# Kernel tuning notes

Hardware: AMD Instinct MI355X
Metric: run time of the kernel (lower is better)

Reference implementation:

```python
import jax, jax.numpy as jnp
import numpy as np

B, L, INPUT_DIM = 4, 4096, 32
D_MODEL, N_LAYERS = 256, 2
D_STATE, D_CONV, EXPAND = 16, 4, 2
D_INNER = EXPAND * D_MODEL          # 512
DT_RANK = (D_MODEL + 15) // 16      # 16
OUTPUT_DIM, HORIZON = 32, 4
LN_EPS = 1e-5


def setup_inputs() -> dict:
    key = jax.random.key(0)
    ks = jax.random.split(key, 16)
    s = 0.02
    inp = {
        "x": jax.random.normal(ks[0], (B, L, INPUT_DIM), jnp.float32),
        "enc_w": jax.random.normal(ks[1], (D_MODEL, INPUT_DIM), jnp.float32) * s,
        "enc_b": jnp.zeros((D_MODEL,), jnp.float32),
        "in_proj_w": jax.random.normal(ks[2], (N_LAYERS, 2 * D_INNER, D_MODEL), jnp.float32) * s,
        "conv_w": jax.random.normal(ks[3], (N_LAYERS, D_INNER, D_CONV), jnp.float32) * s,
        "conv_b": jnp.zeros((N_LAYERS, D_INNER), jnp.float32),
        "xproj_w": jax.random.normal(ks[4], (N_LAYERS, DT_RANK + 2 * D_STATE, D_INNER), jnp.float32) * s,
        "dtproj_w": jax.random.normal(ks[5], (N_LAYERS, D_INNER, DT_RANK), jnp.float32) * s,
        "dtproj_b": jax.random.normal(ks[6], (N_LAYERS, D_INNER), jnp.float32) * 0.1,
        "A_log": jnp.log(jnp.tile(jnp.arange(1.0, D_STATE + 1.0, dtype=jnp.float32), (N_LAYERS, D_INNER, 1))),
        "Dp": jnp.ones((N_LAYERS, D_INNER), jnp.float32),
        "out_proj_w": jax.random.normal(ks[7], (N_LAYERS, D_MODEL, D_INNER), jnp.float32) * s,
        "ln_g": jnp.ones((D_MODEL,), jnp.float32),
        "ln_b": jnp.zeros((D_MODEL,), jnp.float32),
        "head_w": jax.random.normal(ks[8], (OUTPUT_DIM * HORIZON, D_MODEL), jnp.float32) * s,
        "head_b": jnp.zeros((OUTPUT_DIM * HORIZON,), jnp.float32),
    }
    return inp


def _mamba_block(x, in_w, cw, cb, xp_w, dt_w, dt_b, A_log, Dp, out_w):
    # x: [B, L, d_model]
    b, l, _ = x.shape
    xz = jnp.einsum("bld,ed->ble", x, in_w)            # [B, L, 2*d_inner]
    xi, res = jnp.split(xz, 2, axis=-1)
    # causal depthwise conv1d (padding=d_conv-1, truncated to L)
    xpad = jnp.pad(xi, ((0, 0), (D_CONV - 1, 0), (0, 0)))
    xi = sum(xpad[:, k:k + l, :] * cw[:, k] for k in range(D_CONV)) + cb
    xi = jax.nn.silu(xi)
    dbl = jnp.einsum("bld,ed->ble", xi, xp_w)           # [B, L, dt_rank+2*d_state]
    dt = dbl[..., :DT_RANK]
    Bm = dbl[..., DT_RANK:DT_RANK + D_STATE]            # [B, L, d_state]
    Cm = dbl[..., DT_RANK + D_STATE:]                   # [B, L, d_state]
    dt = jax.nn.softplus(jnp.einsum("blr,dr->bld", dt, dt_w) + dt_b)  # [B, L, d_inner]
    A = -jnp.exp(A_log)                                 # [d_inner, d_state]

    def step(h, ins):
        dt_t, B_t, C_t, x_t = ins                       # [B,di],[B,ds],[B,ds],[B,di]
        dA = jnp.exp(dt_t[..., None] * A)               # [B, d_inner, d_state]
        h = dA * h + (dt_t * x_t)[..., None] * B_t[:, None, :]
        y = jnp.einsum("bds,bs->bd", h, C_t)
        return h, y

    h0 = jnp.zeros((b, D_INNER, D_STATE), x.dtype)
    xs = (jnp.moveaxis(dt, 1, 0), jnp.moveaxis(Bm, 1, 0),
          jnp.moveaxis(Cm, 1, 0), jnp.moveaxis(xi, 1, 0))
    _, ys = jax.lax.scan(step, h0, xs)                  # ys: [L, B, d_inner]
    y = jnp.moveaxis(ys, 0, 1) + xi * Dp
    y = y * jax.nn.silu(res)
    return jnp.einsum("ble,de->bld", y, out_w)


def reference(x, enc_w, enc_b, in_proj_w, conv_w, conv_b, xproj_w, dtproj_w,
              dtproj_b, A_log, Dp, out_proj_w, ln_g, ln_b, head_w, head_b):
    h = jnp.einsum("bli,di->bld", x, enc_w) + enc_b     # encoder
    for i in range(N_LAYERS):
        h = h + _mamba_block(h, in_proj_w[i], conv_w[i], conv_b[i], xproj_w[i],
                             dtproj_w[i], dtproj_b[i], A_log[i], Dp[i], out_proj_w[i])
    mu = jnp.mean(h, axis=-1, keepdims=True)
    var = jnp.mean((h - mu) ** 2, axis=-1, keepdims=True)
    hn = (h - mu) * jax.lax.rsqrt(var + LN_EPS) * ln_g + ln_b
    state = hn[:, -1, :]                                # last timestep
    return jnp.einsum("bd,od->bo", state, head_w) + head_b
```

## Files before the change

kernel.cpp:

```cpp
#include <hip/hip_runtime.h>
#include <hip/hip_bf16.h>
#include <math.h>

#define BB 4
#define LL 4096
#define DM 256
#define DI 512
#define DS 16
#define NOUTK 128
#define LN_EPS 1e-5f
#define NC 128
#define CLEN (LL/NC)
#define BL (BB*LL)
#define LDB 640

typedef __attribute__((ext_vector_type(8))) short short8;
typedef __attribute__((ext_vector_type(4))) float f32x4;

__device__ __forceinline__ ushort f2bf(float f) {
    union { float f; unsigned u; } v; v.f = f;
    unsigned r = (v.u + 0x7FFF + ((v.u >> 16) & 1)) >> 16;
    return (ushort)r;
}
__device__ __forceinline__ float bf2f(ushort u) {
    union { unsigned u; float f; } v; v.u = ((unsigned)u) << 16;
    return v.f;
}

#define PREP_N1 (2*1024*256)
#define PREP_N2 (2*256*512)
#define PREP_N3 (2*640*512)
__global__ __launch_bounds__(256) void prep_kernel(
    const float* __restrict__ inw, const float* __restrict__ opw,
    const float* __restrict__ xpw, const float* __restrict__ dtw,
    ushort* __restrict__ inw_bf, ushort* __restrict__ opw_bf,
    ushort* __restrict__ comb_bf)
{
    int i = blockIdx.x * 256 + threadIdx.x;
    if (i < PREP_N1) {
        inw_bf[i] = f2bf(inw[i]);
        return;
    }
    int j = i - PREP_N1;
    if (j < PREP_N2) {
        opw_bf[j] = f2bf(opw[j]);
        return;
    }
    int m = j - PREP_N2;
    if (m >= PREP_N3) return;
    int l = m / (640 * 512);
    int rem = m - l * 640 * 512;
    int row = rem >> 9, k = rem & 511;
    const float* xp = xpw + l * 48 * 512;
    const float* dw = dtw + l * 512 * 16;
    float v;
    if (row < 512) {
        v = 0.f;
        #pragma unroll
        for (int r = 0; r < 16; ++r)
            v = fmaf(dw[row * 16 + r], xp[r * 512 + k], v);
    } else if (row < 544) {
        v = xp[(row - 512 + 16) * 512 + k];
    } else v = 0.f;
    comb_bf[m] = f2bf(v);
}

__global__ __launch_bounds__(256) void enc_kernel(
    const float* __restrict__ x, const float* __restrict__ w,
    const float* __restrict__ b, ushort* __restrict__ hbf)
{
    __shared__ float sw[256 * 33];
    __shared__ float sx[4][32];
    int tid = threadIdx.x;
    for (int i = tid; i < 256 * 8; i += 256) {
        float4 v = ((const float4*)w)[i];
        int r = i >> 3, c = (i & 7) * 4;
        sw[r * 33 + c + 0] = v.x; sw[r * 33 + c + 1] = v.y;
        sw[r * 33 + c + 2] = v.z; sw[r * 33 + c + 3] = v.w;
    }
    int row0 = blockIdx.x * 4;
    if (tid < 32) {
        for (int rr = 0; rr < 4; ++rr)
            sx[rr][tid] = x[(size_t)(row0 + rr) * 32 + tid];
    }
    __syncthreads();
    float bb = b[tid];
    #pragma unroll
    for (int rr = 0; rr < 4; ++rr) {
        float acc = bb;
        #pragma unroll
        for (int k = 0; k < 32; ++k)
            acc = fmaf(sx[rr][k], sw[tid * 33 + k], acc);
        hbf[(size_t)(row0 + rr) * DM + tid] = f2bf(acc);
    }
}

template<int EPI>
__global__ __launch_bounds__(256, 4) void mfma_gemm(
    const ushort* __restrict__ A, int lda,
    const ushort* __restrict__ W,
    const float* __restrict__ bias,
    float* __restrict__ C, int ldc,
    ushort* Cbf, int ldcbf,
    int K)
{
    __shared__ ushort As[64 * 64];
    __shared__ ushort Ws[128 * 64];
    const int tid = threadIdx.x;

    int nwg = gridDim.x * gridDim.y;
    int wlin = blockIdx.y * gridDim.x + blockIdx.x;
    int gx = blockIdx.x, gy = blockIdx.y;
    if ((nwg & 7) == 0) {
        int q = nwg >> 3;
        int s = (wlin & 7) * q + (wlin >> 3);
        gx = s % gridDim.x;
        gy = s / gridDim.x;
    }
    const int bm = gy * 64;
    const int bn = gx * 128;
    const int wid = tid >> 6, lane = tid & 63;
    const int wrow = (wid >> 1) * 32, wcol = (wid & 1) * 64;
    const int sr = tid >> 3;
    const int sc = tid & 7;

    f32x4 acc[2][4];
    #pragma unroll
    for (int mi = 0; mi < 2; ++mi)
        #pragma unroll
        for (int ni = 0; ni < 4; ++ni)
            acc[mi][ni] = (f32x4){0.f, 0.f, 0.f, 0.f};

    const int nk = K >> 6;
    for (int t = 0; t < nk; ++t) {
        const int k0 = t << 6;
        #pragma unroll
        for (int it = 0; it < 2; ++it) {
            int r = it * 32 + sr;
            int csrc = sc ^ (r & 7);
            __builtin_amdgcn_global_load_lds(
                (const __attribute__((address_space(1))) unsigned int*)
                    (A + (size_t)(bm + r) * lda + k0 + csrc * 8),
                (__attribute__((address_space(3))) unsigned int*)
                    (As + r * 64 + sc * 8), 16, 0, 0);
        }
        #pragma unroll
        for (int it = 0; it < 4; ++it) {
            int r = it * 32 + sr;
            int csrc = sc ^ (r & 7);
            __builtin_amdgcn_global_load_lds(
                (const __attribute__((address_space(1))) unsigned int*)
                    (W + (size_t)(bn + r) * K + k0 + csrc * 8),
                (__attribute__((address_space(3))) unsigned int*)
                    (Ws + r * 64 + sc * 8), 16, 0, 0);
        }
        __syncthreads();
        #pragma unroll
        for (int kk = 0; kk < 2; ++kk) {
            short8 af[2], bfr[4];
            #pragma unroll
            for (int mi = 0; mi < 2; ++mi) {
                int r = wrow + mi * 16 + (lane & 15);
                int c = (lane >> 4) + kk * 4;
                af[mi] = *(const short8*)(As + r * 64 + ((c ^ (r & 7)) << 3));
            }
            #pragma unroll
            for (int ni = 0; ni < 4; ++ni) {
                int r = wcol + ni * 16 + (lane & 15);
                int c = (lane >> 4) + kk * 4;
                bfr[ni] = *(const short8*)(Ws + r * 64 + ((c ^ (r & 7)) << 3));
            }
            #pragma unroll
            for (int mi = 0; mi < 2; ++mi)
                #pragma unroll
                for (int ni = 0; ni < 4; ++ni)
                    acc[mi][ni] = __builtin_amdgcn_mfma_f32_16x16x32_bf16(
                        af[mi], bfr[ni], acc[mi][ni], 0, 0, 0);
        }
        __syncthreads();
    }

    #pragma unroll
    for (int mi = 0; mi < 2; ++mi)
        #pragma unroll
        for (int ni = 0; ni < 4; ++ni) {
            int col = bn + wcol + ni * 16 + (lane & 15);
            #pragma unroll
            for (int r = 0; r < 4; ++r) {
                int row = bm + wrow + mi * 16 + (lane >> 4) * 4 + r;
                float v = acc[mi][ni][r];
                if (EPI == 1) {
                    if (col < 512) {
                        float u = v + bias[col];
                        float sp = fmaxf(u, 0.f) + __logf(1.f + __expf(-fabsf(u)));
                        Cbf[(size_t)row * ldcbf + col] = f2bf(sp);
                    } else if (col < 544) {
                        C[(size_t)row * ldc + (col - 512)] = v;
                    }
                } else if (EPI == 2) {
                    size_t o = (size_t)row * ldcbf + col;
                    float vv = v + bf2f(Cbf[o]);
                    Cbf[o] = f2bf(vv);
                } else {
                    Cbf[(size_t)row * ldcbf + col] = f2bf(v);
                }
            }
        }
}

__global__ __launch_bounds__(256) void conv_silu_kernel(
    const ushort* __restrict__ xz, const float* __restrict__ cw,
    const float* __restrict__ cb, ushort* __restrict__ xi)
{
    int idx = blockIdx.x * 256 + threadIdx.x;
    int d4 = (idx & 127) * 4;
    int grp = idx >> 7;
    int b = grp >> 9;
    int t0 = (grp & 511) * 8;
    const ushort* base = xz + ((size_t)(b * LL + t0) * 1024) + d4;
    ushort* obase = xi + ((size_t)(b * LL + t0) * 512) + d4;

    float4 w0 = *(const float4*)(cw + (d4 + 0) * 4);
    float4 w1 = *(const float4*)(cw + (d4 + 1) * 4);
    float4 w2 = *(const float4*)(cw + (d4 + 2) * 4);
    float4 w3 = *(const float4*)(cw + (d4 + 3) * 4);
    float b0 = cb[d4 + 0], b1 = cb[d4 + 1], b2 = cb[d4 + 2], b3 = cb[d4 + 3];

    ushort4 z4 = {0, 0, 0, 0};
    ushort4 win0 = (t0 >= 3) ? *(const ushort4*)(base - 3 * 1024) : z4;
    ushort4 win1 = (t0 >= 2) ? *(const ushort4*)(base - 2 * 1024) : z4;
    ushort4 win2 = (t0 >= 1) ? *(const ushort4*)(base - 1 * 1024) : z4;

    #pragma unroll
    for (int k = 0; k < 8; ++k) {
        ushort4 cur = *(const ushort4*)(base + k * 1024);
        float a0 = b0, a1 = b1, a2 = b2, a3 = b3;
        a0 = fmaf(bf2f(win0.x), w0.x, a0); a1 = fmaf(bf2f(win0.y), w1.x, a1);
        a2 = fmaf(bf2f(win0.z), w2.x, a2); a3 = fmaf(bf2f(win0.w), w3.x, a3);
        a0 = fmaf(bf2f(win1.x), w0.y, a0); a1 = fmaf(bf2f(win1.y), w1.y, a1);
        a2 = fmaf(bf2f(win1.z), w2.y, a2); a3 = fmaf(bf2f(win1.w), w3.y, a3);
        a0 = fmaf(bf2f(win2.x), w0.z, a0); a1 = fmaf(bf2f(win2.y), w1.z, a1);
        a2 = fmaf(bf2f(win2.z), w2.z, a2); a3 = fmaf(bf2f(win2.w), w3.z, a3);
        a0 = fmaf(bf2f(cur.x),  w0.w, a0); a1 = fmaf(bf2f(cur.y),  w1.w, a1);
        a2 = fmaf(bf2f(cur.z),  w2.w, a2); a3 = fmaf(bf2f(cur.w),  w3.w, a3);
        ushort4 o;
        o.x = f2bf(a0 / (1.f + __expf(-a0)));
        o.y = f2bf(a1 / (1.f + __expf(-a1)));
        o.z = f2bf(a2 / (1.f + __expf(-a2)));
        o.w = f2bf(a3 / (1.f + __expf(-a3)));
        *(ushort4*)(obase + k * 512) = o;
        win0 = win1; win1 = win2; win2 = cur;
    }
}

__global__ __launch_bounds__(256) void scan_phase1(
    const ushort* __restrict__ xi, const ushort* __restrict__ dtb,
    const float* __restrict__ bc,
    const float* __restrict__ alog,
    float* __restrict__ cS, float* __restrict__ cH)
{
    int d = blockIdx.z * 256 + threadIdx.x;
    int b = blockIdx.y, c = blockIdx.x;
    float Av[16];
    bool fast = true;
    #pragma unroll
    for (int s = 0; s < 16; ++s) {
        Av[s] = -__expf(alog[d * 16 + s]);
        fast = fast && (fabsf(Av[s] + (float)(s + 1)) < 1e-3f * (s + 1));
    }
    float h[16];
    #pragma unroll
    for (int s = 0; s < 16; ++s) h[s] = 0.f;
    float S = 0.f;
    int t0 = c * CLEN;
    if (fast) {
        for (int t = t0; t < t0 + CLEN; ++t) {
            size_t row = (size_t)b * LL + t;
            float dt = bf2f(dtb[row * 512 + d]);
            float x = bf2f(xi[row * 512 + d]);
            float dtx = dt * x;
            S += dt;
            const float* bp = bc + row * 32;
            float e1 = __expf(-dt);
            float e2=e1*e1, e3=e2*e1, e4=e2*e2, e5=e3*e2, e6=e3*e3, e7=e4*e3, e8=e4*e4;
            float e9=e5*e4, e10=e5*e5, e11=e6*e5, e12=e6*e6, e13=e7*e6, e14=e7*e7, e15=e8*e7, e16=e8*e8;
            float pw[16] = {e1,e2,e3,e4,e5,e6,e7,e8,e9,e10,e11,e12,e13,e14,e15,e16};
            #pragma unroll
            for (int s = 0; s < 16; ++s)
                h[s] = fmaf(pw[s], h[s], dtx * bp[s]);
        }
    } else {
        for (int t = t0; t < t0 + CLEN; ++t) {
            size_t row = (size_t)b * LL + t;
            float dt = bf2f(dtb[row * 512 + d]);
            float x = bf2f(xi[row * 512 + d]);
            float dtx = dt * x;
            S += dt;
            const float* bp = bc + row * 32;
            #pragma unroll
            for (int s = 0; s < 16; ++s) {
                float dA = __expf(dt * Av[s]);
                h[s] = fmaf(dA, h[s], dtx * bp[s]);
            }
        }
    }
    cS[((size_t)b * DI + d) * NC + c] = S;
    size_t base = (((size_t)b * DI + d) * NC + c) * 16;
    #pragma unroll
    for (int q = 0; q < 4; ++q)
        *(float4*)(cH + base + q*4) = *(float4*)&h[q*4];
}

__global__ __launch_bounds__(256) void scan_phase2(
    const float* __restrict__ cS, float* __restrict__ cH,
    const float* __restrict__ alog)
{
    int bd = blockIdx.x;
    int d = bd & (DI - 1);
    int tid = threadIdx.x;
    int s = tid >> 4;
    int g = tid & 15;
    float Avs = -__expf(alog[d * 16 + s]);
    size_t sbase = (size_t)bd * NC;
    size_t base = (size_t)bd * NC * 16 + s;
    float a8[8], h8[8];
    #pragma unroll
    for (int j = 0; j < 8; ++j) {
        float Sj = cS[sbase + g * 8 + j];
        a8[j] = __expf(Avs * Sj);
        h8[j] = cH[base + (size_t)(g * 8 + j) * 16];
    }
    float A = 1.f, H = 0.f;
    #pragma unroll
    for (int j = 0; j < 8; ++j) {
        H = fmaf(a8[j], H, h8[j]);
        A *= a8[j];
    }
    #pragma unroll
    for (int off = 1; off < 16; off <<= 1) {
        float Ap = __shfl_up(A, off, 16);
        float Hp = __shfl_up(H, off, 16);
        if (g >= off) { H = fmaf(A, Hp, H); A *= Ap; }
    }
    float init = __shfl_up(H, 1, 16);
    if (g == 0) init = 0.f;
    #pragma unroll
    for (int j = 0; j < 8; ++j) {
        size_t o = base + (size_t)(g * 8 + j) * 16;
        cH[o] = init;
        init = fmaf(a8[j], init, h8[j]);
    }
}

__global__ __launch_bounds__(256) void scan_phase3(
    const ushort* __restrict__ xz,
    ushort* __restrict__ xi,
    const ushort* __restrict__ dtb,
    const float* __restrict__ bc,
    const float* __restrict__ alog,
    const float* __restrict__ Dp,
    const float* __restrict__ cH,
    int c0)
{
    int d = blockIdx.z * 256 + threadIdx.x;
    int b = blockIdx.y;
    int c = blockIdx.x + c0;
    float Av[16];
    bool fast = true;
    #pragma unroll
    for (int s = 0; s < 16; ++s) {
        Av[s] = -__expf(alog[d * 16 + s]);
        fast = fast && (fabsf(Av[s] + (float)(s + 1)) < 1e-3f * (s + 1));
    }
    float h[16];
    size_t cbase = (((size_t)b * DI + d) * NC + c) * 16;
    #pragma unroll
    for (int q = 0; q < 4; ++q)
        *(float4*)&h[q*4] = *(const float4*)(cH + cbase + q*4);
    float Dd = Dp[d];
    int t0 = c * CLEN;
    if (fast) {
        for (int t = t0; t < t0 + CLEN; ++t) {
            size_t row = (size_t)b * LL + t;
            float dt = bf2f(dtb[row * 512 + d]);
            float x = bf2f(xi[row * 512 + d]);
            float dtx = dt * x;
            const float* bp = bc + row * 32;
            const float* cp = bc + row * 32 + 16;
            float e1 = __expf(-dt);
            float e2=e1*e1, e3=e2*e1, e4=e2*e2, e5=e3*e2, e6=e3*e3, e7=e4*e3, e8=e4*e4;
            float e9=e5*e4, e10=e5*e5, e11=e6*e5, e12=e6*e6, e13=e7*e6, e14=e7*e7, e15=e8*e7, e16=e8*e8;
            float pw[16] = {e1,e2,e3,e4,e5,e6,e7,e8,e9,e10,e11,e12,e13,e14,e15,e16};
            float y = 0.f;
            #pragma unroll
            for (int s = 0; s < 16; ++s) {
                h[s] = fmaf(pw[s], h[s], dtx * bp[s]);
                y = fmaf(h[s], cp[s], y);
            }
            float res = bf2f(xz[row * 1024 + 512 + d]);
            float g = (y + x * Dd) * (res / (1.f + __expf(-res)));
            xi[row * 512 + d] = f2bf(g);
        }
    } else {
        for (int t = t0; t < t0 + CLEN; ++t) {
            size_t row = (size_t)b * LL + t;
            float dt = bf2f(dtb[row * 512 + d]);
            float x = bf2f(xi[row * 512 + d]);
            float dtx = dt * x;
            const float* bp = bc + row * 32;
            const float* cp = bc + row * 32 + 16;
            float y = 0.f;
            #pragma unroll
            for (int s = 0; s < 16; ++s) {
                float dA = __expf(dt * Av[s]);
                h[s] = fmaf(dA, h[s], dtx * bp[s]);
                y = fmaf(h[s], cp[s], y);
            }
            float res = bf2f(xz[row * 1024 + 512 + d]);
            float g = (y + x * Dd) * (res / (1.f + __expf(-res)));
            xi[row * 512 + d] = f2bf(g);
        }
    }
}

__global__ __launch_bounds__(256) void out_proj_last_kernel(
    const ushort* __restrict__ xi, const float* __restrict__ W,
    const ushort* __restrict__ hbf, float* __restrict__ hlast)
{
    int b = blockIdx.x, n = threadIdx.x;
    __shared__ float sy[DI];
    const ushort* yrow = xi + ((size_t)b * LL + (LL - 1)) * DI;
    for (int k = threadIdx.x; k < DI; k += 256) sy[k] = bf2f(yrow[k]);
    __syncthreads();
    const float* wr = W + (size_t)n * DI;
    float acc = 0.f;
    for (int k = 0; k < DI; k += 4) {
        float4 wv = *(const float4*)(wr + k);
        acc = fmaf(sy[k+0], wv.x, acc);
        acc = fmaf(sy[k+1], wv.y, acc);
        acc = fmaf(sy[k+2], wv.z, acc);
        acc = fmaf(sy[k+3], wv.w, acc);
    }
    hlast[b * DM + n] = acc + bf2f(hbf[((size_t)b * LL + (LL - 1)) * DM + n]);
}

__global__ __launch_bounds__(256) void ln_head_kernel(
    const float* __restrict__ hlast, const float* __restrict__ lng,
    const float* __restrict__ lnb, const float* __restrict__ hw,
    const float* __restrict__ hb, float* __restrict__ out)
{
    int b = blockIdx.x, tid = threadIdx.x;
    __shared__ float sh[DM];
    __shared__ float r1[4], r2[4];
    float v = hlast[b * DM + tid];
    float s = v;
    #pragma unroll
    for (int o = 32; o >= 1; o >>= 1) s += __shfl_down(s, o);
    if ((tid & 63) == 0) r1[tid >> 6] = s;
    __syncthreads();
    float mu = (r1[0] + r1[1] + r1[2] + r1[3]) * (1.f / 256.f);
    float dv = v - mu;
    float q = dv * dv;
    #pragma unroll
    for (int o = 32; o >= 1; o >>= 1) q += __shfl_down(q, o);
    if ((tid & 63) == 0) r2[tid >> 6] = q;
    __syncthreads();
    float var = (r2[0] + r2[1] + r2[2] + r2[3]) * (1.f / 256.f);
    sh[tid] = dv * rsqrtf(var + LN_EPS) * lng[tid] + lnb[tid];
    __syncthreads();
    if (tid < NOUTK) {
        const float* wr = hw + (size_t)tid * DM;
        float acc = hb[tid];
        for (int d2 = 0; d2 < DM; d2 += 4) {
            float4 wv = *(const float4*)(wr + d2);
            acc = fmaf(sh[d2+0], wv.x, acc);
            acc = fmaf(sh[d2+1], wv.y, acc);
            acc = fmaf(sh[d2+2], wv.z, acc);
            acc = fmaf(sh[d2+3], wv.w, acc);
        }
        out[b * NOUTK + tid] = acc;
    }
}

extern "C" void kernel_launch(void* const* d_in, const int* in_sizes, int n_in,
                              void* d_out, int out_size, void* d_ws, size_t ws_size,
                              hipStream_t stream)
{
    const float* x    = (const float*)d_in[0];
    const float* encw = (const float*)d_in[1];
    const float* encb = (const float*)d_in[2];
    const float* inw  = (const float*)d_in[3];
    const float* cw   = (const float*)d_in[4];
    const float* cb   = (const float*)d_in[5];
    const float* xpw  = (const float*)d_in[6];
    const float* dtw  = (const float*)d_in[7];
    const float* dtb  = (const float*)d_in[8];
    const float* alog = (const float*)d_in[9];
    const float* Dp   = (const float*)d_in[10];
    const float* opw  = (const float*)d_in[11];
    const float* lng  = (const float*)d_in[12];
    const float* lnb  = (const float*)d_in[13];
    const float* hw   = (const float*)d_in[14];
    const float* hb   = (const float*)d_in[15];
    float* out = (float*)d_out;

    float* ws   = (float*)d_ws;
    float* bc   = ws;
    float* cS   = bc  + (size_t)BL * 32;
    float* cH   = cS  + (size_t)BB * DI * NC;
    float* hlast = cH + (size_t)BB * DI * NC * DS;
    ushort* h_bf    = (ushort*)(hlast + BB * DM);
    ushort* xz_bf   = h_bf  + (size_t)BL * DM;
    ushort* xi_bf   = xz_bf + (size_t)BL * 1024;
    ushort* dt_bf   = xi_bf + (size_t)BL * DI;
    ushort* inw_bf  = dt_bf + (size_t)BL * DI;
    ushort* opw_bf  = inw_bf + 2 * 1024 * DM;
    ushort* comb_bf = opw_bf + 2 * DM * DI;

    dim3 blk(256, 1, 1);

    prep_kernel<<<dim3((PREP_N1 + PREP_N2 + PREP_N3) / 256), blk, 0, stream>>>(
        inw, opw, xpw, dtw, inw_bf, opw_bf, comb_bf);

    enc_kernel<<<dim3(BL/4), blk, 0, stream>>>(x, encw, encb, h_bf);

    for (int l = 0; l < 2; ++l) {
        mfma_gemm<0><<<dim3(1024/128, BL/64), blk, 0, stream>>>(
            h_bf, DM, inw_bf + (size_t)l * 1024 * DM, nullptr,
            nullptr, 0, xz_bf, 1024, DM);
        conv_silu_kernel<<<dim3(BL * 128 / 8 / 256), blk, 0, stream>>>(
            xz_bf, cw + l * DI * 4, cb + l * DI, xi_bf);
        mfma_gemm<1><<<dim3(LDB/128, BL/64), blk, 0, stream>>>(
            xi_bf, DI, comb_bf + (size_t)l * LDB * DI, dtb + l * DI,
            bc, 32, dt_bf, 512, DI);
        scan_phase1<<<dim3(NC, BB, 2), blk, 0, stream>>>(
            xi_bf, dt_bf, bc, alog + (size_t)l * DI * 16, cS, cH);
        scan_phase2<<<dim3(BB * DI), blk, 0, stream>>>(
            cS, cH, alog + (size_t)l * DI * 16);
        if (l == 0) {
            scan_phase3<<<dim3(NC, BB, 2), blk, 0, stream>>>(
                xz_bf, xi_bf, dt_bf, bc, alog + (size_t)l * DI * 16,
                Dp + l * DI, cH, 0);
            mfma_gemm<2><<<dim3(DM/128, BL/64), blk, 0, stream>>>(
                xi_bf, DI, opw_bf + (size_t)l * DM * DI, nullptr,
                nullptr, 0, h_bf, DM, DI);
        } else {
            scan_phase3<<<dim3(1, BB, 2), blk, 0, stream>>>(
                xz_bf, xi_bf, dt_bf, bc, alog + (size_t)l * DI * 16,
                Dp + l * DI, cH, NC - 1);
            out_proj_last_kernel<<<dim3(BB), blk, 0, stream>>>(
                xi_bf, opw + (size_t)l * DM * DI, h_bf, hlast);
        }
    }

    ln_head_kernel<<<dim3(BB), blk, 0, stream>>>(hlast, lng, lnb, hw, hb, out);
}
```

Measured before the change: 306.6 us.

## Load GEMM fragments directly from global memory, dropping LDS staging

The MFMA GEMM no longer stages A and W tiles through LDS with swizzled global_load_lds and barriers. Each wave now reads its bf16 MFMA fragments straight from global memory, and the K loop is fully unrolled through a template parameter. This removes the LDS traffic and the __syncthreads barriers, and the occupancy hint is dropped from launch_bounds. In exchange, tiles shared between waves are reloaded, relying on L1/L2 hits, and the per-lane 16-byte loads with row strides may coalesce less well.

```diff
diff --git a/kernel.cpp b/kernel.cpp
--- a/kernel.cpp
+++ b/kernel.cpp
@@ -95,17 +95,14 @@
     }
 }
 
-template<int EPI>
-__global__ __launch_bounds__(256, 4) void mfma_gemm(
+template<int EPI, int KK>
+__global__ __launch_bounds__(256) void mfma_gemm(
     const ushort* __restrict__ A, int lda,
     const ushort* __restrict__ W,
     const float* __restrict__ bias,
     float* __restrict__ C, int ldc,
-    ushort* Cbf, int ldcbf,
-    int K)
-{
-    __shared__ ushort As[64 * 64];
-    __shared__ ushort Ws[128 * 64];
+    ushort* Cbf, int ldcbf)
+{
     const int tid = threadIdx.x;
 
     int nwg = gridDim.x * gridDim.y;
@@ -121,8 +118,8 @@
     const int bn = gx * 128;
     const int wid = tid >> 6, lane = tid & 63;
     const int wrow = (wid >> 1) * 32, wcol = (wid & 1) * 64;
-    const int sr = tid >> 3;
-    const int sc = tid & 7;
+    const int lr = lane & 15;
+    const int lc = (lane >> 4) * 8;
 
     f32x4 acc[2][4];
     #pragma unroll
@@ -131,53 +128,30 @@
         for (int ni = 0; ni < 4; ++ni)
             acc[mi][ni] = (f32x4){0.f, 0.f, 0.f, 0.f};
 
-    const int nk = K >> 6;
-    for (int t = 0; t < nk; ++t) {
-        const int k0 = t << 6;
-        #pragma unroll
-        for (int it = 0; it < 2; ++it) {
-            int r = it * 32 + sr;
-            int csrc = sc ^ (r & 7);
-            __builtin_amdgcn_global_load_lds(
-                (const __attribute__((address_space(1))) unsigned int*)
-                    (A + (size_t)(bm + r) * lda + k0 + csrc * 8),
-                (__attribute__((address_space(3))) unsigned int*)
-                    (As + r * 64 + sc * 8), 16, 0, 0);
-        }
-        #pragma unroll
-        for (int it = 0; it < 4; ++it) {
-            int r = it * 32 + sr;
-            int csrc = sc ^ (r & 7);
-            __builtin_amdgcn_global_load_lds(
-                (const __attribute__((address_space(1))) unsigned int*)
-                    (W + (size_t)(bn + r) * K + k0 + csrc * 8),
-                (__attribute__((address_space(3))) unsigned int*)
-                    (Ws + r * 64 + sc * 8), 16, 0, 0);
-        }
-        __syncthreads();
-        #pragma unroll
-        for (int kk = 0; kk < 2; ++kk) {
-            short8 af[2], bfr[4];
-            #pragma unroll
-            for (int mi = 0; mi < 2; ++mi) {
-                int r = wrow + mi * 16 + (lane & 15);
-                int c = (lane >> 4) + kk * 4;
-                af[mi] = *(const short8*)(As + r * 64 + ((c ^ (r & 7)) << 3));
-            }
-            #pragma unroll
-            for (int ni = 0; ni < 4; ++ni) {
-                int r = wcol + ni * 16 + (lane & 15);
-                int c = (lane >> 4) + kk * 4;
-                bfr[ni] = *(const short8*)(Ws + r * 64 + ((c ^ (r & 7)) << 3));
-            }
-            #pragma unroll
-            for (int mi = 0; mi < 2; ++mi)
-                #pragma unroll
-                for (int ni = 0; ni < 4; ++ni)
-                    acc[mi][ni] = __builtin_amdgcn_mfma_f32_16x16x32_bf16(
-                        af[mi], bfr[ni], acc[mi][ni], 0, 0, 0);
-        }
-        __syncthreads();
+    const ushort* a0 = A + (size_t)(bm + wrow + lr) * lda + lc;
+    const ushort* a1 = a0 + (size_t)16 * lda;
+    const ushort* w0 = W + (size_t)(bn + wcol + lr) * KK + lc;
+    const ushort* w1 = w0 + 16 * KK;
+    const ushort* w2 = w0 + 32 * KK;
+    const ushort* w3 = w0 + 48 * KK;
+
+    #pragma unroll
+    for (int ks = 0; ks < KK / 32; ++ks) {
+        const int ko = ks * 32;
+        short8 af0 = *(const short8*)(a0 + ko);
+        short8 af1 = *(const short8*)(a1 + ko);
+        short8 b0  = *(const short8*)(w0 + ko);
+        short8 b1  = *(const short8*)(w1 + ko);
+        short8 b2  = *(const short8*)(w2 + ko);
+        short8 b3  = *(const short8*)(w3 + ko);
+        acc[0][0] = __builtin_amdgcn_mfma_f32_16x16x32_bf16(af0, b0, acc[0][0], 0, 0, 0);
+        acc[0][1] = __builtin_amdgcn_mfma_f32_16x16x32_bf16(af0, b1, acc[0][1], 0, 0, 0);
+        acc[0][2] = __builtin_amdgcn_mfma_f32_16x16x32_bf16(af0, b2, acc[0][2], 0, 0, 0);
+        acc[0][3] = __builtin_amdgcn_mfma_f32_16x16x32_bf16(af0, b3, acc[0][3], 0, 0, 0);
+        acc[1][0] = __builtin_amdgcn_mfma_f32_16x16x32_bf16(af1, b0, acc[1][0], 0, 0, 0);
+        acc[1][1] = __builtin_amdgcn_mfma_f32_16x16x32_bf16(af1, b1, acc[1][1], 0, 0, 0);
+        acc[1][2] = __builtin_amdgcn_mfma_f32_16x16x32_bf16(af1, b2, acc[1][2], 0, 0, 0);
+        acc[1][3] = __builtin_amdgcn_mfma_f32_16x16x32_bf16(af1, b3, acc[1][3], 0, 0, 0);
     }
 
     #pragma unroll
@@ -525,14 +499,14 @@
     enc_kernel<<<dim3(BL/4), blk, 0, stream>>>(x, encw, encb, h_bf);
 
     for (int l = 0; l < 2; ++l) {
-        mfma_gemm<0><<<dim3(1024/128, BL/64), blk, 0, stream>>>(
+        mfma_gemm<0, DM><<<dim3(1024/128, BL/64), blk, 0, stream>>>(
             h_bf, DM, inw_bf + (size_t)l * 1024 * DM, nullptr,
-            nullptr, 0, xz_bf, 1024, DM);
+            nullptr, 0, xz_bf, 1024);
         conv_silu_kernel<<<dim3(BL * 128 / 8 / 256), blk, 0, stream>>>(
             xz_bf, cw + l * DI * 4, cb + l * DI, xi_bf);
-        mfma_gemm<1><<<dim3(LDB/128, BL/64), blk, 0, stream>>>(
+        mfma_gemm<1, DI><<<dim3(LDB/128, BL/64), blk, 0, stream>>>(
             xi_bf, DI, comb_bf + (size_t)l * LDB * DI, dtb + l * DI,
-            bc, 32, dt_bf, 512, DI);
+            bc, 32, dt_bf, 512);
         scan_phase1<<<dim3(NC, BB, 2), blk, 0, stream>>>(
             xi_bf, dt_bf, bc, alog + (size_t)l * DI * 16, cS, cH);
         scan_phase2<<<dim3(BB * DI), blk, 0, stream>>>(
@@ -541,9 +515,9 @@
             scan_phase3<<<dim3(NC, BB, 2), blk, 0, stream>>>(
                 xz_bf, xi_bf, dt_bf, bc, alog + (size_t)l * DI * 16,
                 Dp + l * DI, cH, 0);
-            mfma_gemm<2><<<dim3(DM/128, BL/64), blk, 0, stream>>>(
+            mfma_gemm<2, DI><<<dim3(DM/128, BL/64), blk, 0, stream>>>(
                 xi_bf, DI, opw_bf + (size_t)l * DM * DI, nullptr,
-                nullptr, 0, h_bf, DM, DI);
+                nullptr, 0, h_bf, DM);
         } else {
             scan_phase3<<<dim3(1, BB, 2), blk, 0, stream>>>(
                 xz_bf, xi_bf, dt_bf, bc, alog + (size_t)l * DI * 16,
```

Result: slower. 473.2 us (+54.3%).
